# Kernel tuning notes

Hardware: AMD Instinct MI355X
Metric: run time of the kernel (lower is better)

The kernel has to match this reference:

```python
import jax, jax.numpy as jnp
import numpy as np
import math

L, H, E, D = 4, 8, 256, 32  # layers, heads, embed, head_dim
SCALE = 1.0 / math.sqrt(D)

def _ln(x, w, b, eps=1e-5):
    mu = jnp.mean(x, -1, keepdims=True)
    var = jnp.mean((x - mu) ** 2, -1, keepdims=True)
    return (x - mu) * jax.lax.rsqrt(var + eps) * w + b

def setup_inputs() -> dict:
    key = jax.random.key(0)
    ks = jax.random.split(key, 16)
    B, S, C = 32, 512, 512
    w = lambda k, sh: jax.random.normal(k, sh, jnp.float32) * 0.05
    return {
        'cnn_features': jax.random.normal(ks[0], (B, S, C), jnp.float32),
        'cnn_w': w(ks[1], (E, C)), 'cnn_b': jnp.zeros((E,), jnp.float32),
        'tok_emb': w(ks[2], (2, E)),
        'Wq': w(ks[3], (L, E, E)), 'bq': jnp.zeros((L, E), jnp.float32),
        'Wk': w(ks[4], (L, E, E)), 'bk': jnp.zeros((L, E), jnp.float32),
        'Wv': w(ks[5], (L, E, E)), 'bv': jnp.zeros((L, E), jnp.float32),
        'Wo': w(ks[6], (L, E, E)), 'bo': jnp.zeros((L, E), jnp.float32),
        'ln1_w': jnp.ones((L, E), jnp.float32), 'ln1_b': jnp.zeros((L, E), jnp.float32),
        'ln2_w': jnp.ones((L, E), jnp.float32), 'ln2_b': jnp.zeros((L, E), jnp.float32),
        'mlp_w1': w(ks[7], (L, 3 * E, E)), 'mlp_b1': jnp.zeros((L, 3 * E), jnp.float32),
        'mlp_w2': w(ks[8], (L, E, 3 * E)), 'mlp_b2': jnp.zeros((L, E), jnp.float32),
        'lnf_w': jnp.ones((E,), jnp.float32), 'lnf_b': jnp.zeros((E,), jnp.float32),
        'out_w1': w(ks[9], (2 * E, E)), 'out_b1': jnp.zeros((2 * E,), jnp.float32),
        'out_w2': w(ks[10], (C, 2 * E)), 'out_b2': jnp.zeros((C,), jnp.float32),
    }

def _forward(cnn_features, cnn_w, cnn_b, tok_emb, Wq, bq, Wk, bk, Wv, bv, Wo, bo,
             ln1_w, ln1_b, ln2_w, ln2_b, mlp_w1, mlp_b1, mlp_w2, mlp_b2,
             lnf_w, lnf_b, out_w1, out_b1, out_w2, out_b2):
    B, S, _ = cnn_features.shape
    # CNN feature projection + token-type embedding (all tokens type 0)
    x = cnn_features @ cnn_w.T + cnn_b + tok_emb[0]  # [B,S,E]
    for i in range(L):
        q = (x @ Wq[i].T + bq[i]).reshape(B, S, H, D).transpose(0, 2, 1, 3)
        k = (x @ Wk[i].T + bk[i]).reshape(B, S, H, D).transpose(0, 2, 1, 3)
        v = (x @ Wv[i].T + bv[i]).reshape(B, S, H, D).transpose(0, 2, 1, 3)
        scores = jnp.einsum('bhqd,bhkd->bhqk', q, k) * SCALE
        attn = jax.nn.softmax(scores, axis=-1)  # dropout = identity (eval)
        attended = jnp.einsum('bhqk,bhkd->bhqd', attn, v)
        attended = attended.transpose(0, 2, 1, 3).reshape(B, S, E)
        attn_out = attended @ Wo[i].T + bo[i]
        x = _ln(x + attn_out, ln1_w[i], ln1_b[i])
        h = jax.nn.gelu(x @ mlp_w1[i].T + mlp_b1[i], approximate=False)
        mlp_out = h @ mlp_w2[i].T + mlp_b2[i]
        x = _ln(x + mlp_out, ln2_w[i], ln2_b[i])
    x = _ln(x, lnf_w, lnf_b)
    h = jax.nn.gelu(x @ out_w1.T + out_b1, approximate=False)
    out = jax.nn.relu(h @ out_w2.T + out_b2)  # [B,S,cnn_feature_dim]
    return out

def reference(cnn_features, cnn_w, cnn_b, tok_emb, Wq, bq, Wk, bk, Wv, bv, Wo, bo,
              ln1_w, ln1_b, ln2_w, ln2_b, mlp_w1, mlp_b1, mlp_w2, mlp_b2,
              lnf_w, lnf_b, out_w1, out_b1, out_w2, out_b2):
    return _forward(cnn_features, cnn_w, cnn_b, tok_emb, Wq, bq, Wk, bk, Wv, bv, Wo, bo,
                    ln1_w, ln1_b, ln2_w, ln2_b, mlp_w1, mlp_b1, mlp_w2, mlp_b2,
                    lnf_w, lnf_b, out_w1, out_b1, out_w2, out_b2)
```

## Files before the change

kernel.cpp:

```cpp
#include <hip/hip_runtime.h>
#include <math.h>

#define B_SZ 32
#define S_SZ 512
#define C_SZ 512
#define E_SZ 256
#define H_SZ 8
#define D_SZ 32
#define L_SZ 4
#define N_TOK (B_SZ * S_SZ)
#define HID 768
#define MB (1048576)

typedef __attribute__((ext_vector_type(8))) short bf16x8;
typedef __attribute__((ext_vector_type(4))) float f32x4_t;

__device__ __forceinline__ float gelu_f(float x) {
    return 0.5f * x * (1.0f + erff(x * 0.70710678118654752f));
}

__device__ __forceinline__ ushort f2bf(float f) {
    uint u = __float_as_uint(f);
    return (ushort)((u + 0x7FFFu + ((u >> 16) & 1u)) >> 16);
}
__device__ __forceinline__ uint pack2(float a, float b) {
    return (uint)f2bf(a) | ((uint)f2bf(b) << 16);
}
__device__ __forceinline__ void unpack8(uint4 u, float* f) {
    f[0] = __uint_as_float((u.x & 0xFFFFu) << 16); f[1] = __uint_as_float(u.x & 0xFFFF0000u);
    f[2] = __uint_as_float((u.y & 0xFFFFu) << 16); f[3] = __uint_as_float(u.y & 0xFFFF0000u);
    f[4] = __uint_as_float((u.z & 0xFFFFu) << 16); f[5] = __uint_as_float(u.z & 0xFFFF0000u);
    f[6] = __uint_as_float((u.w & 0xFFFFu) << 16); f[7] = __uint_as_float(u.w & 0xFFFF0000u);
}

__global__ __launch_bounds__(256)
void cvt_kernel(const float* __restrict__ src, ushort* __restrict__ dst)
{
    const int i = (blockIdx.x * 256 + threadIdx.x) * 8;
    const float4 a = *(const float4*)(src + i);
    const float4 b = *(const float4*)(src + i + 4);
    uint4 o;
    o.x = pack2(a.x, a.y); o.y = pack2(a.z, a.w);
    o.z = pack2(b.x, b.y); o.w = pack2(b.z, b.w);
    *(uint4*)(dst + i) = o;
}

__global__ __launch_bounds__(256)
void bqkv_kernel(const float* __restrict__ bq, const float* __restrict__ bk,
                 const float* __restrict__ bv, float* __restrict__ dst)
{
    const int idx = blockIdx.x * 256 + threadIdx.x;
    const int layer = idx / 768, j = idx % 768;
    float v = (j < 256) ? bq[layer * 256 + j]
            : (j < 512) ? bk[layer * 256 + j - 256]
                        : bv[layer * 256 + j - 512];
    dst[layer * 768 + j] = v;
}

template<int ACT, int EPI, bool OF, bool OB>
__global__ __launch_bounds__(256)
void gemm_bf16_kernel(const ushort* __restrict__ A, const ushort* __restrict__ W,
                      const float* __restrict__ bias, const float* __restrict__ bias2,
                      float* __restrict__ Cf, ushort* __restrict__ Cb,
                      ushort* __restrict__ Cb2, int M, int K, int F)
{
    constexpr int LDT = 40;
    __shared__ __align__(16) ushort As[128 * LDT];
    __shared__ __align__(16) ushort Bs[64 * LDT];
    const int tid = threadIdx.x;
    const int bm = blockIdx.x * 128, bn = blockIdx.y * 64;
    const int ar = tid >> 2, aks = tid & 3;

    uint4 pa0, pa1, pb;
    {
        pa0 = *(const uint4*)(A + (size_t)(bm + ar) * K + aks * 8);
        pa1 = *(const uint4*)(A + (size_t)(bm + ar + 64) * K + aks * 8);
        pb  = *(const uint4*)(W + (size_t)(bn + ar) * K + aks * 8);
    }

    const int lane = tid & 63, w = tid >> 6;
    const int wm = w >> 1, wn = w & 1;
    const int fr = lane & 15, fk = lane >> 4;
    f32x4_t acc[4][2] = {};

    for (int k0 = 0;;) {
        __syncthreads();
        *(uint4*)&As[ar * LDT + aks * 8] = pa0;
        *(uint4*)&As[(ar + 64) * LDT + aks * 8] = pa1;
        *(uint4*)&Bs[ar * LDT + aks * 8] = pb;
        __syncthreads();
        k0 += 32;
        if (k0 < K) {
            pa0 = *(const uint4*)(A + (size_t)(bm + ar) * K + k0 + aks * 8);
            pa1 = *(const uint4*)(A + (size_t)(bm + ar + 64) * K + k0 + aks * 8);
            pb  = *(const uint4*)(W + (size_t)(bn + ar) * K + k0 + aks * 8);
        }
        bf16x8 af[4], bw[2];
        #pragma unroll
        for (int i = 0; i < 4; ++i)
            af[i] = *(const bf16x8*)&As[(wm * 64 + i * 16 + fr) * LDT + fk * 8];
        #pragma unroll
        for (int j = 0; j < 2; ++j)
            bw[j] = *(const bf16x8*)&Bs[(wn * 32 + j * 16 + fr) * LDT + fk * 8];
        #pragma unroll
        for (int i = 0; i < 4; ++i)
            #pragma unroll
            for (int j = 0; j < 2; ++j)
                acc[i][j] = __builtin_amdgcn_mfma_f32_16x16x32_bf16(af[i], bw[j], acc[i][j], 0, 0, 0);
        if (k0 >= K) break;
    }

    #pragma unroll
    for (int j = 0; j < 2; ++j) {
        const int col = bn + wn * 32 + j * 16 + fr;
        float bb = bias[col];
        if (bias2) bb += bias2[col];
        #pragma unroll
        for (int i = 0; i < 4; ++i) {
            #pragma unroll
            for (int r = 0; r < 4; ++r) {
                const int row = bm + wm * 64 + i * 16 + fk * 4 + r;
                float t = acc[i][j][r] + bb;
                if (ACT == 1) t = gelu_f(t);
                if (ACT == 2) t = fmaxf(t, 0.0f);
                if (EPI == 1) {
                    const int b2 = row >> 9, s2 = row & 511;
                    if (col < 512) {
                        Cb[(size_t)row * 512 + col] = f2bf(t);
                    } else {
                        const int cc = col - 512;
                        Cb2[(size_t)(((b2 << 3) + (cc >> 5)) << 14) + ((cc & 31) << 9) + s2] = f2bf(t);
                    }
                } else {
                    if (OF) Cf[(size_t)row * F + col] = t;
                    if (OB) Cb[(size_t)row * F + col] = f2bf(t);
                }
            }
        }
    }
}

__global__ __launch_bounds__(256)
void attn_v3(const ushort* __restrict__ qk, const ushort* __restrict__ vt,
             ushort* __restrict__ out)
{
    __shared__ __align__(16) ushort Ks[128 * 40];
    __shared__ __align__(16) ushort Vs[32 * 168];
    const int bh = blockIdx.x, qc = blockIdx.y;
    const int b = bh >> 3, h = bh & 7;
    const int tid = threadIdx.x;
    const int w = tid >> 6, lane = tid & 63;
    const int g = lane >> 4, c = lane & 15;
    const size_t qrow = (size_t)b * 512 + qc * 64 + w * 16;

    bf16x8 qf;
    {
        const uint4 qv = *(const uint4*)(qk + (qrow + c) * 512 + h * 32 + g * 8);
        float f[8]; unpack8(qv, f);
        const float scale = 0.17677669529663689f;
        union { uint u[4]; bf16x8 v; } qq;
        #pragma unroll
        for (int j = 0; j < 4; ++j) qq.u[j] = pack2(f[2*j] * scale, f[2*j+1] * scale);
        qf = qq.v;
    }

    float m = -INFINITY, l = 0.f;
    f32x4_t o0 = {0.f, 0.f, 0.f, 0.f}, o1 = {0.f, 0.f, 0.f, 0.f};
    const f32x4_t zz = {0.f, 0.f, 0.f, 0.f};

    for (int kt = 0; kt < 4; ++kt) {
        __syncthreads();
        #pragma unroll
        for (int i = 0; i < 2; ++i) {
            const int idx = tid + i * 256;
            const int kr = idx >> 2, seg = idx & 3;
            const uint4 kv = *(const uint4*)(qk + ((size_t)b * 512 + kt * 128 + kr) * 512
                                             + 256 + h * 32 + seg * 8);
            const int p = (((kr >> 2) & 1) << 4) | (((kr >> 3) & 3) << 2) | (kr & 3);
            const int pos = (kr & ~31) | p;
            *(uint4*)&Ks[pos * 40 + seg * 8] = kv;
        }
        #pragma unroll
        for (int i = 0; i < 2; ++i) {
            const int idx = tid + i * 256;
            const int dr = idx >> 4, seg = idx & 15;
            const uint4 vv = *(const uint4*)(vt + (size_t)bh * 16384 + dr * 512
                                             + kt * 128 + seg * 8);
            *(uint4*)&Vs[dr * 168 + seg * 8] = vv;
        }
        __syncthreads();

        f32x4_t s[8];
        #pragma unroll
        for (int kf = 0; kf < 8; ++kf) {
            const bf16x8 kfrag = *(const bf16x8*)&Ks[(kf * 16 + c) * 40 + g * 8];
            s[kf] = __builtin_amdgcn_mfma_f32_16x16x32_bf16(kfrag, qf, zz, 0, 0, 0);
        }

        float mt = s[0][0];
        #pragma unroll
        for (int kf = 0; kf < 8; ++kf)
            #pragma unroll
            for (int r = 0; r < 4; ++r) mt = fmaxf(mt, s[kf][r]);
        mt = fmaxf(mt, __shfl_xor(mt, 16));
        mt = fmaxf(mt, __shfl_xor(mt, 32));
        const float mn = fmaxf(m, mt);
        const float corr = __expf(m - mn);
        m = mn;
        float lt = 0.f;
        #pragma unroll
        for (int kf = 0; kf < 8; ++kf)
            #pragma unroll
            for (int r = 0; r < 4; ++r) {
                const float p = __expf(s[kf][r] - mn);
                s[kf][r] = p; lt += p;
            }
        lt += __shfl_xor(lt, 16);
        lt += __shfl_xor(lt, 32);
        l = l * corr + lt;
        #pragma unroll
        for (int r = 0; r < 4; ++r) { o0[r] *= corr; o1[r] *= corr; }

        #pragma unroll
        for (int t = 0; t < 4; ++t) {
            union { uint u[4]; bf16x8 v; } pf;
            pf.u[0] = pack2(s[2*t][0],   s[2*t][1]);
            pf.u[1] = pack2(s[2*t][2],   s[2*t][3]);
            pf.u[2] = pack2(s[2*t+1][0], s[2*t+1][1]);
            pf.u[3] = pack2(s[2*t+1][2], s[2*t+1][3]);
            const bf16x8 va0 = *(const bf16x8*)&Vs[(0 * 16 + c) * 168 + t * 32 + g * 8];
            const bf16x8 va1 = *(const bf16x8*)&Vs[(1 * 16 + c) * 168 + t * 32 + g * 8];
            o0 = __builtin_amdgcn_mfma_f32_16x16x32_bf16(va0, pf.v, o0, 0, 0, 0);
            o1 = __builtin_amdgcn_mfma_f32_16x16x32_bf16(va1, pf.v, o1, 0, 0, 0);
        }
    }

    const float inv = 1.0f / l;
    const size_t obase = (qrow + c) * 256 + h * 32;
    #pragma unroll
    for (int r = 0; r < 4; ++r) {
        out[obase + g * 4 + r]      = f2bf(o0[r] * inv);
        out[obase + 16 + g * 4 + r] = f2bf(o1[r] * inv);
    }
}

__global__ __launch_bounds__(256)
void add_ln2_kernel(float* __restrict__ x, const float* __restrict__ resid,
                    const float* __restrict__ w, const float* __restrict__ b,
                    ushort* __restrict__ xb)
{
    const int lane = threadIdx.x & 63;
    const int wv = threadIdx.x >> 6;
    const size_t row = (size_t)blockIdx.x * 4 + wv;
    float4 val = *(const float4*)(x + row * E_SZ + lane * 4);
    if (resid) {
        const float4 r = *(const float4*)(resid + row * E_SZ + lane * 4);
        val.x += r.x; val.y += r.y; val.z += r.z; val.w += r.w;
    }
    float s  = val.x + val.y + val.z + val.w;
    float ss = val.x * val.x + val.y * val.y + val.z * val.z + val.w * val.w;
    #pragma unroll
    for (int off = 1; off < 64; off <<= 1) {
        s  += __shfl_xor(s, off, 64);
        ss += __shfl_xor(ss, off, 64);
    }
    const float mu  = s * (1.0f / 256.0f);
    const float var = ss * (1.0f / 256.0f) - mu * mu;
    const float rs  = rsqrtf(var + 1e-5f);
    const float4 wv4 = *(const float4*)(w + lane * 4);
    const float4 bv4 = *(const float4*)(b + lane * 4);
    float4 o;
    o.x = (val.x - mu) * rs * wv4.x + bv4.x;
    o.y = (val.y - mu) * rs * wv4.y + bv4.y;
    o.z = (val.z - mu) * rs * wv4.z + bv4.z;
    o.w = (val.w - mu) * rs * wv4.w + bv4.w;
    *(float4*)(x + row * E_SZ + lane * 4) = o;
    ushort4 ob;
    ob.x = f2bf(o.x); ob.y = f2bf(o.y); ob.z = f2bf(o.z); ob.w = f2bf(o.w);
    *(ushort4*)(xb + row * E_SZ + lane * 4) = ob;
}

extern "C" void kernel_launch(void* const* d_in, const int* in_sizes, int n_in,
                              void* d_out, int out_size, void* d_ws, size_t ws_size,
                              hipStream_t stream)
{
    const float* cnn   = (const float*)d_in[0];
    const float* cnn_w = (const float*)d_in[1];
    const float* cnn_b = (const float*)d_in[2];
    const float* tok   = (const float*)d_in[3];
    const float* Wq    = (const float*)d_in[4];
    const float* bq    = (const float*)d_in[5];
    const float* Wk    = (const float*)d_in[6];
    const float* bk    = (const float*)d_in[7];
    const float* Wv    = (const float*)d_in[8];
    const float* bv    = (const float*)d_in[9];
    const float* Wo    = (const float*)d_in[10];
    const float* bo    = (const float*)d_in[11];
    const float* ln1w  = (const float*)d_in[12];
    const float* ln1b  = (const float*)d_in[13];
    const float* ln2w  = (const float*)d_in[14];
    const float* ln2b  = (const float*)d_in[15];
    const float* mw1   = (const float*)d_in[16];
    const float* mb1   = (const float*)d_in[17];
    const float* mw2   = (const float*)d_in[18];
    const float* mb2   = (const float*)d_in[19];
    const float* lnfw  = (const float*)d_in[20];
    const float* lnfb  = (const float*)d_in[21];
    const float* ow1   = (const float*)d_in[22];
    const float* ob1   = (const float*)d_in[23];
    const float* ow2   = (const float*)d_in[24];
    const float* ob2   = (const float*)d_in[25];

    const int M = N_TOK;
    char* ws = (char*)d_ws;

    float*  x     = (float*)(ws + 0);
    ushort* xb    = (ushort*)(ws + 16 * MB);
    ushort* qkb   = (ushort*)(ws + 24 * MB);
    float*  resid = (float*)(ws + 24 * MB);
    ushort* cnnb  = (ushort*)(ws + 24 * MB);
    ushort* vt    = (ushort*)(ws + 40 * MB);
    ushort* ab_   = (ushort*)(ws + 48 * MB);
    ushort* hb_   = (ushort*)(ws + 40 * MB);
    ushort* wb    = (ushort*)(ws + 64 * MB);

    ushort* cnn_wb = wb;
    ushort* Wob    = wb + 131072;
    ushort* wqkv   = wb + 393216;
    ushort* mw1b   = wb + 1179648;
    ushort* mw2b   = wb + 1966080;
    ushort* ow1b   = wb + 2752512;
    ushort* ow2b   = wb + 2883584;
    float*  bqkv   = (float*)(ws + 64 * MB + 6291456);

    cvt_kernel<<<dim3(4096), dim3(256), 0, stream>>>(cnn, cnnb);
    cvt_kernel<<<dim3(64),  dim3(256), 0, stream>>>(cnn_w, cnn_wb);
    cvt_kernel<<<dim3(128), dim3(256), 0, stream>>>(Wo, Wob);
    cvt_kernel<<<dim3(384), dim3(256), 0, stream>>>(mw1, mw1b);
    cvt_kernel<<<dim3(384), dim3(256), 0, stream>>>(mw2, mw2b);
    cvt_kernel<<<dim3(64),  dim3(256), 0, stream>>>(ow1, ow1b);
    cvt_kernel<<<dim3(128), dim3(256), 0, stream>>>(ow2, ow2b);
    for (int i = 0; i < L_SZ; ++i) {
        cvt_kernel<<<dim3(32), dim3(256), 0, stream>>>(Wq + (size_t)i * 65536, wqkv + (size_t)i * 196608);
        cvt_kernel<<<dim3(32), dim3(256), 0, stream>>>(Wk + (size_t)i * 65536, wqkv + (size_t)i * 196608 + 65536);
        cvt_kernel<<<dim3(32), dim3(256), 0, stream>>>(Wv + (size_t)i * 65536, wqkv + (size_t)i * 196608 + 131072);
    }
    bqkv_kernel<<<dim3(12), dim3(256), 0, stream>>>(bq, bk, bv, bqkv);

    gemm_bf16_kernel<0, 0, true, true><<<dim3(M / 128, E_SZ / 64), dim3(256), 0, stream>>>(
        cnnb, cnn_wb, cnn_b, tok, x, xb, nullptr, M, C_SZ, E_SZ);

    for (int i = 0; i < L_SZ; ++i) {
        gemm_bf16_kernel<0, 1, false, false><<<dim3(M / 128, HID / 64), dim3(256), 0, stream>>>(
            xb, wqkv + (size_t)i * 196608, bqkv + (size_t)i * 768, nullptr,
            nullptr, qkb, vt, M, E_SZ, HID);

        attn_v3<<<dim3(B_SZ * H_SZ, S_SZ / 64), dim3(256), 0, stream>>>(qkb, vt, ab_);

        gemm_bf16_kernel<0, 0, true, false><<<dim3(M / 128, E_SZ / 64), dim3(256), 0, stream>>>(
            ab_, Wob + (size_t)i * 65536, bo + (size_t)i * E_SZ, nullptr,
            resid, nullptr, nullptr, M, E_SZ, E_SZ);
        add_ln2_kernel<<<dim3(M / 4), dim3(256), 0, stream>>>(
            x, resid, ln1w + (size_t)i * E_SZ, ln1b + (size_t)i * E_SZ, xb);

        gemm_bf16_kernel<1, 0, false, true><<<dim3(M / 128, HID / 64), dim3(256), 0, stream>>>(
            xb, mw1b + (size_t)i * HID * E_SZ, mb1 + (size_t)i * HID, nullptr,
            nullptr, hb_, nullptr, M, E_SZ, HID);
        gemm_bf16_kernel<0, 0, true, false><<<dim3(M / 128, E_SZ / 64), dim3(256), 0, stream>>>(
            hb_, mw2b + (size_t)i * E_SZ * HID, mb2 + (size_t)i * E_SZ, nullptr,
            resid, nullptr, nullptr, M, HID, E_SZ);
        add_ln2_kernel<<<dim3(M / 4), dim3(256), 0, stream>>>(
            x, resid, ln2w + (size_t)i * E_SZ, ln2b + (size_t)i * E_SZ, xb);
    }

    add_ln2_kernel<<<dim3(M / 4), dim3(256), 0, stream>>>(x, nullptr, lnfw, lnfb, xb);

    gemm_bf16_kernel<1, 0, false, true><<<dim3(M / 128, (2 * E_SZ) / 64), dim3(256), 0, stream>>>(
        xb, ow1b, ob1, nullptr, nullptr, hb_, nullptr, M, E_SZ, 2 * E_SZ);
    gemm_bf16_kernel<2, 0, true, false><<<dim3(M / 128, C_SZ / 64), dim3(256), 0, stream>>>(
        hb_, ow2b, ob2, nullptr, (float*)d_out, nullptr, nullptr, M, 2 * E_SZ, C_SZ);
}
```

Before: 592.8 us.

## Double-buffer GEMM with direct global-to-LDS loads, prefetch attention tiles, merge QKV converts

The GEMM now uses global_load_lds to write A/W tiles straight into double-buffered, XOR-swizzled LDS, so the next K-tile loads while MFMAs run. The attention kernel register-prefetches the next K/V tile and raises wave priority around its MFMA blocks. The twelve per-layer QKV weight conversion launches are merged into one kernel, and pack2 now uses the hardware bf16 conversion intrinsic. Risks: the swizzle and LDS-load lane mapping must be exactly right, and the extra prefetch registers may lower attention occupancy.

```diff
diff --git a/kernel.cpp b/kernel.cpp
--- a/kernel.cpp
+++ b/kernel.cpp
@@ -1,4 +1,5 @@
 #include <hip/hip_runtime.h>
+#include <hip/hip_bf16.h>
 #include <math.h>
 
 #define B_SZ 32
@@ -24,13 +25,21 @@
     return (ushort)((u + 0x7FFFu + ((u >> 16) & 1u)) >> 16);
 }
 __device__ __forceinline__ uint pack2(float a, float b) {
-    return (uint)f2bf(a) | ((uint)f2bf(b) << 16);
+    __hip_bfloat162 h = __float22bfloat162_rn(make_float2(a, b));
+    union { __hip_bfloat162 h; uint u; } c; c.h = h;
+    return c.u;
 }
 __device__ __forceinline__ void unpack8(uint4 u, float* f) {
     f[0] = __uint_as_float((u.x & 0xFFFFu) << 16); f[1] = __uint_as_float(u.x & 0xFFFF0000u);
     f[2] = __uint_as_float((u.y & 0xFFFFu) << 16); f[3] = __uint_as_float(u.y & 0xFFFF0000u);
     f[4] = __uint_as_float((u.z & 0xFFFFu) << 16); f[5] = __uint_as_float(u.z & 0xFFFF0000u);
     f[6] = __uint_as_float((u.w & 0xFFFFu) << 16); f[7] = __uint_as_float(u.w & 0xFFFF0000u);
+}
+
+__device__ __forceinline__ void gload16(const ushort* g, ushort* l) {
+    __builtin_amdgcn_global_load_lds(
+        (const __attribute__((address_space(1))) void*)g,
+        (__attribute__((address_space(3))) void*)l, 16, 0, 0);
 }
 
 __global__ __launch_bounds__(256)
@@ -46,6 +55,23 @@
 }
 
 __global__ __launch_bounds__(256)
+void wqkv_cvt_kernel(const float* __restrict__ Wq, const float* __restrict__ Wk,
+                     const float* __restrict__ Wv, ushort* __restrict__ dst)
+{
+    const int i = (blockIdx.x * 256 + threadIdx.x) * 8;
+    const int layer = i / 196608;
+    const int rem = i - layer * 196608;
+    const int sub = rem >> 16, off = rem & 65535;
+    const float* src = (sub == 0 ? Wq : sub == 1 ? Wk : Wv) + layer * 65536 + off;
+    const float4 a = *(const float4*)src;
+    const float4 b = *(const float4*)(src + 4);
+    uint4 o;
+    o.x = pack2(a.x, a.y); o.y = pack2(a.z, a.w);
+    o.z = pack2(b.x, b.y); o.w = pack2(b.z, b.w);
+    *(uint4*)(dst + i) = o;
+}
+
+__global__ __launch_bounds__(256)
 void bqkv_kernel(const float* __restrict__ bq, const float* __restrict__ bk,
                  const float* __restrict__ bv, float* __restrict__ dst)
 {
@@ -64,50 +90,51 @@
                       float* __restrict__ Cf, ushort* __restrict__ Cb,
                       ushort* __restrict__ Cb2, int M, int K, int F)
 {
-    constexpr int LDT = 40;
-    __shared__ __align__(16) ushort As[128 * LDT];
-    __shared__ __align__(16) ushort Bs[64 * LDT];
+    __shared__ __align__(16) ushort As[2][128 * 32];
+    __shared__ __align__(16) ushort Bs[2][64 * 32];
     const int tid = threadIdx.x;
     const int bm = blockIdx.x * 128, bn = blockIdx.y * 64;
-    const int ar = tid >> 2, aks = tid & 3;
-
-    uint4 pa0, pa1, pb;
-    {
-        pa0 = *(const uint4*)(A + (size_t)(bm + ar) * K + aks * 8);
-        pa1 = *(const uint4*)(A + (size_t)(bm + ar + 64) * K + aks * 8);
-        pb  = *(const uint4*)(W + (size_t)(bn + ar) * K + aks * 8);
-    }
-
     const int lane = tid & 63, w = tid >> 6;
+    const int lr = lane >> 2, ls = lane & 3;
+    const int lsx = ls ^ ((lr >> 1) & 3);
     const int wm = w >> 1, wn = w & 1;
     const int fr = lane & 15, fk = lane >> 4;
+    const int rseg = (fk ^ ((fr >> 1) & 3)) * 8;
     f32x4_t acc[4][2] = {};
 
-    for (int k0 = 0;;) {
-        __syncthreads();
-        *(uint4*)&As[ar * LDT + aks * 8] = pa0;
-        *(uint4*)&As[(ar + 64) * LDT + aks * 8] = pa1;
-        *(uint4*)&Bs[ar * LDT + aks * 8] = pb;
-        __syncthreads();
-        k0 += 32;
-        if (k0 < K) {
-            pa0 = *(const uint4*)(A + (size_t)(bm + ar) * K + k0 + aks * 8);
-            pa1 = *(const uint4*)(A + (size_t)(bm + ar + 64) * K + k0 + aks * 8);
-            pb  = *(const uint4*)(W + (size_t)(bn + ar) * K + k0 + aks * 8);
+    const ushort* Ag0 = A + (size_t)(bm + w * 32 + lr) * K + lsx * 8;
+    const ushort* Ag1 = Ag0 + (size_t)16 * K;
+    const ushort* Wg  = W + (size_t)(bn + w * 16 + lr) * K + lsx * 8;
+    const int la0 = (w * 32) * 32, la1 = (w * 32 + 16) * 32, lb = (w * 16) * 32;
+
+    gload16(Ag0, &As[0][la0]);
+    gload16(Ag1, &As[0][la1]);
+    gload16(Wg,  &Bs[0][lb]);
+    __syncthreads();
+
+    const int NT = K >> 5;
+    int cur = 0;
+    for (int t = 0; t < NT; ++t) {
+        if (t + 1 < NT) {
+            const int k0 = (t + 1) << 5;
+            gload16(Ag0 + k0, &As[cur ^ 1][la0]);
+            gload16(Ag1 + k0, &As[cur ^ 1][la1]);
+            gload16(Wg  + k0, &Bs[cur ^ 1][lb]);
         }
         bf16x8 af[4], bw[2];
         #pragma unroll
         for (int i = 0; i < 4; ++i)
-            af[i] = *(const bf16x8*)&As[(wm * 64 + i * 16 + fr) * LDT + fk * 8];
+            af[i] = *(const bf16x8*)&As[cur][(wm * 64 + i * 16 + fr) * 32 + rseg];
         #pragma unroll
         for (int j = 0; j < 2; ++j)
-            bw[j] = *(const bf16x8*)&Bs[(wn * 32 + j * 16 + fr) * LDT + fk * 8];
+            bw[j] = *(const bf16x8*)&Bs[cur][(wn * 32 + j * 16 + fr) * 32 + rseg];
         #pragma unroll
         for (int i = 0; i < 4; ++i)
             #pragma unroll
             for (int j = 0; j < 2; ++j)
                 acc[i][j] = __builtin_amdgcn_mfma_f32_16x16x32_bf16(af[i], bw[j], acc[i][j], 0, 0, 0);
-        if (k0 >= K) break;
+        __syncthreads();
+        cur ^= 1;
     }
 
     #pragma unroll
@@ -164,6 +191,15 @@
         qf = qq.v;
     }
 
+    uint4 pk[2], pv[2];
+    #pragma unroll
+    for (int i = 0; i < 2; ++i) {
+        const int idx = tid + i * 256;
+        pk[i] = *(const uint4*)(qk + ((size_t)b * 512 + (idx >> 2)) * 512
+                                + 256 + h * 32 + (idx & 3) * 8);
+        pv[i] = *(const uint4*)(vt + (size_t)bh * 16384 + (idx >> 4) * 512 + (idx & 15) * 8);
+    }
+
     float m = -INFINITY, l = 0.f;
     f32x4_t o0 = {0.f, 0.f, 0.f, 0.f}, o1 = {0.f, 0.f, 0.f, 0.f};
     const f32x4_t zz = {0.f, 0.f, 0.f, 0.f};
@@ -174,28 +210,32 @@
         for (int i = 0; i < 2; ++i) {
             const int idx = tid + i * 256;
             const int kr = idx >> 2, seg = idx & 3;
-            const uint4 kv = *(const uint4*)(qk + ((size_t)b * 512 + kt * 128 + kr) * 512
-                                             + 256 + h * 32 + seg * 8);
             const int p = (((kr >> 2) & 1) << 4) | (((kr >> 3) & 3) << 2) | (kr & 3);
             const int pos = (kr & ~31) | p;
-            *(uint4*)&Ks[pos * 40 + seg * 8] = kv;
-        }
-        #pragma unroll
-        for (int i = 0; i < 2; ++i) {
-            const int idx = tid + i * 256;
-            const int dr = idx >> 4, seg = idx & 15;
-            const uint4 vv = *(const uint4*)(vt + (size_t)bh * 16384 + dr * 512
-                                             + kt * 128 + seg * 8);
-            *(uint4*)&Vs[dr * 168 + seg * 8] = vv;
+            *(uint4*)&Ks[pos * 40 + seg * 8] = pk[i];
+            const int dr = idx >> 4, vseg = idx & 15;
+            *(uint4*)&Vs[dr * 168 + vseg * 8] = pv[i];
         }
         __syncthreads();
+        if (kt < 3) {
+            #pragma unroll
+            for (int i = 0; i < 2; ++i) {
+                const int idx = tid + i * 256;
+                pk[i] = *(const uint4*)(qk + ((size_t)b * 512 + (kt + 1) * 128 + (idx >> 2)) * 512
+                                        + 256 + h * 32 + (idx & 3) * 8);
+                pv[i] = *(const uint4*)(vt + (size_t)bh * 16384 + (idx >> 4) * 512
+                                        + (kt + 1) * 128 + (idx & 15) * 8);
+            }
+        }
 
         f32x4_t s[8];
+        __builtin_amdgcn_s_setprio(1);
         #pragma unroll
         for (int kf = 0; kf < 8; ++kf) {
             const bf16x8 kfrag = *(const bf16x8*)&Ks[(kf * 16 + c) * 40 + g * 8];
             s[kf] = __builtin_amdgcn_mfma_f32_16x16x32_bf16(kfrag, qf, zz, 0, 0, 0);
         }
+        __builtin_amdgcn_s_setprio(0);
 
         float mt = s[0][0];
         #pragma unroll
@@ -230,8 +270,10 @@
             pf.u[3] = pack2(s[2*t+1][2], s[2*t+1][3]);
             const bf16x8 va0 = *(const bf16x8*)&Vs[(0 * 16 + c) * 168 + t * 32 + g * 8];
             const bf16x8 va1 = *(const bf16x8*)&Vs[(1 * 16 + c) * 168 + t * 32 + g * 8];
+            __builtin_amdgcn_s_setprio(1);
             o0 = __builtin_amdgcn_mfma_f32_16x16x32_bf16(va0, pf.v, o0, 0, 0, 0);
             o1 = __builtin_amdgcn_mfma_f32_16x16x32_bf16(va1, pf.v, o1, 0, 0, 0);
+            __builtin_amdgcn_s_setprio(0);
         }
     }
 
@@ -340,11 +382,7 @@
     cvt_kernel<<<dim3(384), dim3(256), 0, stream>>>(mw2, mw2b);
     cvt_kernel<<<dim3(64),  dim3(256), 0, stream>>>(ow1, ow1b);
     cvt_kernel<<<dim3(128), dim3(256), 0, stream>>>(ow2, ow2b);
-    for (int i = 0; i < L_SZ; ++i) {
-        cvt_kernel<<<dim3(32), dim3(256), 0, stream>>>(Wq + (size_t)i * 65536, wqkv + (size_t)i * 196608);
-        cvt_kernel<<<dim3(32), dim3(256), 0, stream>>>(Wk + (size_t)i * 65536, wqkv + (size_t)i * 196608 + 65536);
-        cvt_kernel<<<dim3(32), dim3(256), 0, stream>>>(Wv + (size_t)i * 65536, wqkv + (size_t)i * 196608 + 131072);
-    }
+    wqkv_cvt_kernel<<<dim3(384), dim3(256), 0, stream>>>(Wq, Wk, Wv, wqkv);
     bqkv_kernel<<<dim3(12), dim3(256), 0, stream>>>(bq, bk, bv, bqkv);
 
     gemm_bf16_kernel<0, 0, true, true><<<dim3(M / 128, E_SZ / 64), dim3(256), 0, stream>>>(
```

After: 689.1 us. 1.16x slower.
